# Kernel optimization log

Measured on AMD Instinct MI355X. Metric: run time of the kernel, lower is better.

## Reference

```python
import jax, jax.numpy as jnp
import numpy as np
from math import sqrt


def setup_inputs() -> dict:
    key = jax.random.key(0)
    k1, k2, k3, k4, k5 = jax.random.split(key, 5)
    B, L, H, D = 16, 4096, 16, 64
    S, M = 4096, 256
    queries = jax.random.normal(k1, (B, L, H, D), dtype=jnp.float32)
    keys = jax.random.normal(k2, (B, S, H, D), dtype=jnp.float32)
    values = jax.random.normal(k3, (B, S, H, D), dtype=jnp.float32)
    # nn.Linear(L_k=S, M): weight [M, S], bias [M]
    squeeze_w = jax.random.normal(k4, (M, S), dtype=jnp.float32) / sqrt(S)
    squeeze_b = jax.random.normal(k5, (M,), dtype=jnp.float32) * 0.01
    return {"queries": queries, "keys": keys, "values": values,
            "squeeze_w": squeeze_w, "squeeze_b": squeeze_b}


def reference(queries, keys, values, squeeze_w, squeeze_b):
    # queries: [B,L,H,D]; keys/values: [B,S,H,D]; squeeze_w: [M,S]; squeeze_b: [M]
    B, L, H, D = queries.shape
    scale = 1.0 / sqrt(D)
    bias = squeeze_b[None, :, None, None]  # broadcast over [B,M,H,D]
    # Linear over the sequence axis S -> M (Linformer compression)
    keys_sq = jnp.einsum('bshd,ms->bmhd', keys, squeeze_w) + bias      # [B,M,H,D]
    values_sq = jnp.einsum('bshd,ms->bmhd', values, squeeze_w) + bias  # [B,M,H,D]
    # Scaled dot-product attention against compressed K/V
    attn = jnp.einsum('blhd,bmhd->bhlm', queries, keys_sq) * scale     # [B,H,L,M]
    attn = jax.nn.softmax(attn, axis=-1)  # dropout is identity in eval / p=0
    context = jnp.einsum('bhlm,bmhd->blhd', attn, values_sq)           # [B,L,H,D]
    return context
```

## Files before the change

kernel.cpp:

```cpp
#include <hip/hip_runtime.h>

#define NB 16
#define NL 4096
#define NH 16
#define ND 64
#define NS 4096
#define NM 256

typedef __fp16 f16;
typedef __attribute__((ext_vector_type(8)))  __fp16 f16x8;
typedef __attribute__((ext_vector_type(4)))  __fp16 f16x4;
typedef __attribute__((ext_vector_type(2)))  __fp16 f16x2;
typedef __attribute__((ext_vector_type(4)))  float  f32x4;
typedef __attribute__((ext_vector_type(16))) float  f32x16;

__device__ __forceinline__ void gload_lds16(const void* g, void* l) {
  __builtin_amdgcn_global_load_lds(
      (const __attribute__((address_space(1))) void*)g,
      (__attribute__((address_space(3))) void*)l, 16, 0, 0);
}

__device__ __forceinline__ int pk2(float a, float b) {
  f16x2 t = __builtin_amdgcn_cvt_pkrtz(a, b);
  union { f16x2 h; int i; } u; u.h = t; return u.i;
}

__global__ __launch_bounds__(256) void k_wcvt(const float* __restrict__ W,
                                              f16* __restrict__ Wk) {
  const int o  = blockIdx.x * 256 + threadIdx.x;
  const int m  = o & 255;
  const int kb = o >> 8;
  const float* src = W + (long)m * NS + kb * 8;
  f32x4 v0 = *(const f32x4*)(src);
  f32x4 v1 = *(const f32x4*)(src + 4);
  union { f16x8 v; f16x2 h2[4]; } pk;
  pk.h2[0] = __builtin_amdgcn_cvt_pkrtz(v0[0], v0[1]);
  pk.h2[1] = __builtin_amdgcn_cvt_pkrtz(v0[2], v0[3]);
  pk.h2[2] = __builtin_amdgcn_cvt_pkrtz(v1[0], v1[1]);
  pk.h2[3] = __builtin_amdgcn_cvt_pkrtz(v1[2], v1[3]);
  *(f16x8*)(Wk + (long)o * 8) = pk.v;
}

__global__ __launch_bounds__(512, 4) void k_squeeze_p(
    const f16* __restrict__ Wk, const float* __restrict__ keys,
    const float* __restrict__ values, float* __restrict__ P) {
  const int h  = blockIdx.x & 15;
  const int b  = (blockIdx.x >> 4) & 15;
  const int sq = (blockIdx.x >> 8) & 1;
  const int t  = blockIdx.x >> 9;
  const float* __restrict__ X = t ? values : keys;

  __shared__ __align__(16) f16 XT0[64 * 72];
  __shared__ __align__(16) f16 XT1[64 * 72];

  const int tid  = threadIdx.x;
  const int lane = tid & 63;
  const int w    = tid >> 6;
  const int l31  = lane & 31;
  const int g    = lane >> 5;

  const int sp = tid & 31;
  const int ng = tid >> 5;
  const float* Xb = X + ((long)b * NS + sq * 2048) * (NH * ND) + h * ND;

  f32x16 acc[2];
#pragma unroll
  for (int di = 0; di < 2; ++di)
#pragma unroll
    for (int r = 0; r < 16; ++r) acc[di][r] = 0.f;

  f32x4 xrA[2], xrB[2];
#pragma unroll
  for (int r = 0; r < 2; ++r)
    xrA[r] = *(const f32x4*)(Xb + (long)(2 * sp + r) * (NH * ND) + ng * 4);
#pragma unroll
  for (int r = 0; r < 2; ++r)
    xrB[r] = *(const f32x4*)(Xb + (long)(64 + 2 * sp + r) * (NH * ND) + ng * 4);

  const f16* Wlane = Wk + ((long)sq * 256 * 256 + (long)g * 256 + w * 32 + l31) * 8;

  for (int kt2 = 0; kt2 < 16; ++kt2) {
    {
      const int kt = 2 * kt2;
      f16x8 af[4];
#pragma unroll
      for (int ks = 0; ks < 4; ++ks)
        af[ks] = *(const f16x8*)(Wlane + ((long)(kt * 8 + ks * 2) * 256) * 8);
      int p0 = pk2(xrA[0][0], xrA[1][0]);
      int p1 = pk2(xrA[0][1], xrA[1][1]);
      int p2 = pk2(xrA[0][2], xrA[1][2]);
      int p3 = pk2(xrA[0][3], xrA[1][3]);
      if (kt2 < 15) {
#pragma unroll
        for (int r = 0; r < 2; ++r)
          xrA[r] = *(const f32x4*)(Xb + (long)((kt + 2) * 64 + 2 * sp + r) * (NH * ND) + ng * 4);
      }
      *(int*)((char*)XT0 + (ng * 4 + 0) * 144 + sp * 4) = p0;
      *(int*)((char*)XT0 + (ng * 4 + 1) * 144 + sp * 4) = p1;
      *(int*)((char*)XT0 + (ng * 4 + 2) * 144 + sp * 4) = p2;
      *(int*)((char*)XT0 + (ng * 4 + 3) * 144 + sp * 4) = p3;
      __syncthreads();
#pragma unroll
      for (int ks = 0; ks < 4; ++ks) {
        f16x8 bf0 = *(const f16x8*)((const char*)XT0 + l31 * 144 + ks * 32 + g * 16);
        f16x8 bf1 = *(const f16x8*)((const char*)XT0 + (32 + l31) * 144 + ks * 32 + g * 16);
        acc[0] = __builtin_amdgcn_mfma_f32_32x32x16_f16(af[ks], bf0, acc[0], 0, 0, 0);
        acc[1] = __builtin_amdgcn_mfma_f32_32x32x16_f16(af[ks], bf1, acc[1], 0, 0, 0);
      }
    }
    {
      const int kt = 2 * kt2 + 1;
      f16x8 af[4];
#pragma unroll
      for (int ks = 0; ks < 4; ++ks)
        af[ks] = *(const f16x8*)(Wlane + ((long)(kt * 8 + ks * 2) * 256) * 8);
      int p0 = pk2(xrB[0][0], xrB[1][0]);
      int p1 = pk2(xrB[0][1], xrB[1][1]);
      int p2 = pk2(xrB[0][2], xrB[1][2]);
      int p3 = pk2(xrB[0][3], xrB[1][3]);
      if (kt2 < 15) {
#pragma unroll
        for (int r = 0; r < 2; ++r)
          xrB[r] = *(const f32x4*)(Xb + (long)((kt + 2) * 64 + 2 * sp + r) * (NH * ND) + ng * 4);
      }
      *(int*)((char*)XT1 + (ng * 4 + 0) * 144 + sp * 4) = p0;
      *(int*)((char*)XT1 + (ng * 4 + 1) * 144 + sp * 4) = p1;
      *(int*)((char*)XT1 + (ng * 4 + 2) * 144 + sp * 4) = p2;
      *(int*)((char*)XT1 + (ng * 4 + 3) * 144 + sp * 4) = p3;
      __syncthreads();
#pragma unroll
      for (int ks = 0; ks < 4; ++ks) {
        f16x8 bf0 = *(const f16x8*)((const char*)XT1 + l31 * 144 + ks * 32 + g * 16);
        f16x8 bf1 = *(const f16x8*)((const char*)XT1 + (32 + l31) * 144 + ks * 32 + g * 16);
        acc[0] = __builtin_amdgcn_mfma_f32_32x32x16_f16(af[ks], bf0, acc[0], 0, 0, 0);
        acc[1] = __builtin_amdgcn_mfma_f32_32x32x16_f16(af[ks], bf1, acc[1], 0, 0, 0);
      }
    }
  }

  const long bh = b * 16 + h;
  float* Pb = P + (((long)t * 256 + bh) * 2 + sq) * (NM * ND);
#pragma unroll
  for (int di = 0; di < 2; ++di) {
    const int d = di * 32 + l31;
#pragma unroll
    for (int rq = 0; rq < 4; ++rq) {
      const int m0 = w * 32 + rq * 8 + g * 4;
      f32x4 st;
      st[0] = acc[di][rq * 4 + 0]; st[1] = acc[di][rq * 4 + 1];
      st[2] = acc[di][rq * 4 + 2]; st[3] = acc[di][rq * 4 + 3];
      *(f32x4*)(Pb + d * 256 + m0) = st;
    }
  }
}

__global__ __launch_bounds__(256) void k_reduce(const float* __restrict__ P,
                                                const float* __restrict__ bias,
                                                f16* __restrict__ Ksq,
                                                f16* __restrict__ Vsq) {
  const int bh = blockIdx.x & 255;
  const int t  = blockIdx.x >> 8;
  const float* P0 = P + (((long)t * 256 + bh) * 2 + 0) * (NM * ND);
  const float* P1 = P + (((long)t * 256 + bh) * 2 + 1) * (NM * ND);
  const int tid = threadIdx.x;

#pragma unroll
  for (int i = 0; i < 16; ++i) {
    const int v = i * 256 + tid;
    const int d = v >> 6;
    const int m = (v & 63) * 4;
    f32x4 a = *(const f32x4*)(P0 + d * 256 + m);
    f32x4 bv = *(const f32x4*)(P1 + d * 256 + m);
    f32x4 bb = *(const f32x4*)(bias + m);
    f32x4 s = a + bv + bb;
    if (t == 0) {
      f16* K = Ksq + (long)bh * (NM * ND);
#pragma unroll
      for (int j = 0; j < 4; ++j)
        K[((d >> 3) * 256 + m + j) * 8 + (d & 7)] = (f16)s[j];
    } else {
      f16* V = Vsq + (long)bh * (ND * NM);
      f16x2 q0 = __builtin_amdgcn_cvt_pkrtz(s[0], s[1]);
      f16x2 q1 = __builtin_amdgcn_cvt_pkrtz(s[2], s[3]);
      f16x4 pv; pv[0] = q0[0]; pv[1] = q0[1]; pv[2] = q1[0]; pv[3] = q1[1];
      *(f16x4*)(V + ((m >> 3) * 64 + d) * 8 + (m & 7)) = pv;
    }
  }
}

__global__ __launch_bounds__(256, 2) void k_attn(const float* __restrict__ Q,
                                                 const f16* __restrict__ Ksq,
                                                 const f16* __restrict__ Vsq,
                                                 float* __restrict__ Out) {
  const int xcd   = blockIdx.x & 7;
  const int local = blockIdx.x >> 3;
  const int bh    = xcd * 32 + (local >> 1);
  const int chunk = local & 1;
  const int b = bh >> 4, h = bh & 15;

  __shared__ __align__(16) f16 Klds[8 * 256 * 8];
  __shared__ __align__(16) f16 Vlds[32 * 64 * 8];

  const int tid = threadIdx.x, lane = tid & 63, w = tid >> 6;
  const int q = lane & 31, hi = lane >> 5;

  const float* Qlane = Q   + (((long)b * NL + q) * NH + h) * ND;
  float*       Olane = Out + (((long)b * NL + q) * NH + h) * ND;
  const float  c = 0.125f * 1.44269504088896f;

  f32x4 qv[8];
  {
    const float* qp = Qlane + (long)(chunk * 2048 + w * 32) * (NH * ND) + hi * 8;
#pragma unroll
    for (int kt = 0; kt < 4; ++kt) {
      qv[2 * kt]     = *(const f32x4*)(qp + kt * 16);
      qv[2 * kt + 1] = *(const f32x4*)(qp + kt * 16 + 4);
    }
  }

  {
    const f16* Kg = Ksq + (long)bh * 16384;
    const f16* Vg = Vsq + (long)bh * 16384;
#pragma unroll
    for (int i = 0; i < 8; ++i)
      gload_lds16(Kg + w * 4096 + i * 512 + lane * 8, (char*)Klds + w * 8192 + i * 1024);
#pragma unroll
    for (int i = 0; i < 8; ++i)
      gload_lds16(Vg + w * 4096 + i * 512 + lane * 8, (char*)Vlds + w * 8192 + i * 1024);
  }
  __syncthreads();

  for (int it = 0; it < 16; ++it) {
    const int row0 = chunk * 2048 + it * 128 + w * 32;

    union { f16x8 v; f16x2 h2[4]; } qb[4];
#pragma unroll
    for (int kt = 0; kt < 4; ++kt) {
      qb[kt].h2[0] = __builtin_amdgcn_cvt_pkrtz(qv[2 * kt][0], qv[2 * kt][1]);
      qb[kt].h2[1] = __builtin_amdgcn_cvt_pkrtz(qv[2 * kt][2], qv[2 * kt][3]);
      qb[kt].h2[2] = __builtin_amdgcn_cvt_pkrtz(qv[2 * kt + 1][0], qv[2 * kt + 1][1]);
      qb[kt].h2[3] = __builtin_amdgcn_cvt_pkrtz(qv[2 * kt + 1][2], qv[2 * kt + 1][3]);
    }

    if (it + 1 < 16) {
      const float* qp = Qlane + (long)(row0 + 128) * (NH * ND) + hi * 8;
#pragma unroll
      for (int kt = 0; kt < 4; ++kt) {
        qv[2 * kt]     = *(const f32x4*)(qp + kt * 16);
        qv[2 * kt + 1] = *(const f32x4*)(qp + kt * 16 + 4);
      }
    }

    f32x16 sa[8];
#pragma unroll
    for (int mf = 0; mf < 8; ++mf)
#pragma unroll
      for (int r = 0; r < 16; ++r) sa[mf][r] = 0.f;

#pragma unroll
    for (int kt = 0; kt < 4; ++kt) {
#pragma unroll
      for (int mf = 0; mf < 8; ++mf) {
        f16x8 ka = *(const f16x8*)((const char*)Klds +
                                   ((2 * kt + hi) * 256 + mf * 32 + q) * 16);
        sa[mf] = __builtin_amdgcn_mfma_f32_32x32x16_f16(ka, qb[kt].v, sa[mf], 0, 0, 0);
      }
    }

    f32x16 mm = sa[0];
#pragma unroll
    for (int mf = 1; mf < 8; ++mf)
#pragma unroll
      for (int r = 0; r < 16; ++r) mm[r] = fmaxf(mm[r], sa[mf][r]);
    float m8_0 = fmaxf(mm[0], mm[8]),  m8_1 = fmaxf(mm[1], mm[9]);
    float m8_2 = fmaxf(mm[2], mm[10]), m8_3 = fmaxf(mm[3], mm[11]);
    float m8_4 = fmaxf(mm[4], mm[12]), m8_5 = fmaxf(mm[5], mm[13]);
    float m8_6 = fmaxf(mm[6], mm[14]), m8_7 = fmaxf(mm[7], mm[15]);
    float mx = fmaxf(fmaxf(fmaxf(m8_0, m8_1), fmaxf(m8_2, m8_3)),
                     fmaxf(fmaxf(m8_4, m8_5), fmaxf(m8_6, m8_7)));
    mx = fmaxf(mx, __shfl_xor(mx, 32));

#pragma unroll
    for (int mf = 0; mf < 8; ++mf)
#pragma unroll
      for (int r = 0; r < 16; ++r)
        sa[mf][r] = __builtin_amdgcn_exp2f((sa[mf][r] - mx) * c);

    f32x16 t0 = sa[0] + sa[1];
    f32x16 t1 = sa[2] + sa[3];
    f32x16 t2 = sa[4] + sa[5];
    f32x16 t3 = sa[6] + sa[7];
    t0 = (t0 + t1) + (t2 + t3);
    float s8_0 = t0[0] + t0[8],  s8_1 = t0[1] + t0[9];
    float s8_2 = t0[2] + t0[10], s8_3 = t0[3] + t0[11];
    float s8_4 = t0[4] + t0[12], s8_5 = t0[5] + t0[13];
    float s8_6 = t0[6] + t0[14], s8_7 = t0[7] + t0[15];
    float sum = ((s8_0 + s8_1) + (s8_2 + s8_3)) + ((s8_4 + s8_5) + (s8_6 + s8_7));
    sum += __shfl_xor(sum, 32);
    const float inv = 1.0f / sum;

    f32x16 o[2];
#pragma unroll
    for (int df = 0; df < 2; ++df)
#pragma unroll
      for (int r = 0; r < 16; ++r) o[df][r] = 0.f;

#pragma unroll
    for (int t = 0; t < 16; ++t) {
      const int fp = t >> 1, s = t & 1;
      int a0 = pk2(sa[fp][8 * s + 0] * inv, sa[fp][8 * s + 1] * inv);
      int a1 = pk2(sa[fp][8 * s + 2] * inv, sa[fp][8 * s + 3] * inv);
      int b0 = pk2(sa[fp][8 * s + 4] * inv, sa[fp][8 * s + 5] * inv);
      int b1 = pk2(sa[fp][8 * s + 6] * inv, sa[fp][8 * s + 7] * inv);
      asm volatile("v_permlane32_swap_b32 %0, %1" : "+v"(a0), "+v"(b0));
      asm volatile("v_permlane32_swap_b32 %0, %1" : "+v"(a1), "+v"(b1));
      union { int w4[4]; f16x8 v; } pb;
      pb.w4[0] = a0; pb.w4[1] = a1; pb.w4[2] = b0; pb.w4[3] = b1;
#pragma unroll
      for (int df = 0; df < 2; ++df) {
        f16x8 va = *(const f16x8*)((const char*)Vlds +
                                   ((2 * t + hi) * 64 + df * 32 + q) * 16);
        o[df] = __builtin_amdgcn_mfma_f32_32x32x16_f16(va, pb.v, o[df], 0, 0, 0);
      }
    }

    float* op = Olane + (long)row0 * (NH * ND);
#pragma unroll
    for (int df = 0; df < 2; ++df)
#pragma unroll
      for (int rq = 0; rq < 4; ++rq) {
        f32x4 st;
        st[0] = o[df][rq * 4 + 0]; st[1] = o[df][rq * 4 + 1];
        st[2] = o[df][rq * 4 + 2]; st[3] = o[df][rq * 4 + 3];
        *(f32x4*)(op + df * 32 + rq * 8 + hi * 4) = st;
      }
  }
}

extern "C" void kernel_launch(void* const* d_in, const int* in_sizes, int n_in,
                              void* d_out, int out_size, void* d_ws, size_t ws_size,
                              hipStream_t stream) {
  const float* Qp   = (const float*)d_in[0];
  const float* Kp   = (const float*)d_in[1];
  const float* Vp   = (const float*)d_in[2];
  const float* Wp   = (const float*)d_in[3];
  const float* bp   = (const float*)d_in[4];
  float*       Outp = (float*)d_out;

  char* ws = (char*)d_ws;
  f16*   Wk  = (f16*)ws;
  f16*   Ksq = (f16*)(ws + (2l << 20));
  f16*   Vsq = (f16*)(ws + (10l << 20));
  float* P   = (float*)(ws + (18l << 20));

  hipLaunchKernelGGL(k_wcvt, dim3(512), dim3(256), 0, stream, Wp, Wk);
  hipLaunchKernelGGL(k_squeeze_p, dim3(1024), dim3(512), 0, stream, Wk, Kp, Vp, P);
  hipLaunchKernelGGL(k_reduce, dim3(512), dim3(256), 0, stream, P, bp, Ksq, Vsq);
  hipLaunchKernelGGL(k_attn, dim3(512), dim3(256), 0, stream, Qp, Ksq, Vsq, Outp);
}
```

Before: 349.5 us.

## Retile squeeze GEMM to cover four heads per block with swizzled LDS

The squeeze kernel now uses 1024-thread blocks, each computing a 256x256 output tile (4 heads x 64 dims) instead of one head. The W fragment each wave loads is reused across 4 MFMA N-fragments, and the X rows are read as contiguous 1 KB chunks. LDS tiles are XOR-swizzled to avoid bank conflicts, and a custom barrier waits only on LDS counters so global prefetches stay in flight. Only 256 blocks are launched and LDS use per block is larger, which lowers occupancy and parallelism. The intermediate P layout and the reduce kernel's indexing change to match.

```diff
diff --git a/kernel.cpp b/kernel.cpp
--- a/kernel.cpp
+++ b/kernel.cpp
@@ -23,6 +23,13 @@
 __device__ __forceinline__ int pk2(float a, float b) {
   f16x2 t = __builtin_amdgcn_cvt_pkrtz(a, b);
   union { f16x2 h; int i; } u; u.h = t; return u.i;
+}
+
+__device__ __forceinline__ void sync_nodrain() {
+  asm volatile("s_waitcnt lgkmcnt(0)" ::: "memory");
+  __builtin_amdgcn_sched_barrier(0);
+  __builtin_amdgcn_s_barrier();
+  __builtin_amdgcn_sched_barrier(0);
 }
 
 __global__ __launch_bounds__(256) void k_wcvt(const float* __restrict__ W,
@@ -41,115 +48,91 @@
   *(f16x8*)(Wk + (long)o * 8) = pk.v;
 }
 
-__global__ __launch_bounds__(512, 4) void k_squeeze_p(
+__global__ __launch_bounds__(1024, 4) void k_squeeze_p(
     const f16* __restrict__ Wk, const float* __restrict__ keys,
     const float* __restrict__ values, float* __restrict__ P) {
-  const int h  = blockIdx.x & 15;
-  const int b  = (blockIdx.x >> 4) & 15;
-  const int sq = (blockIdx.x >> 8) & 1;
-  const int t  = blockIdx.x >> 9;
+  const int sq = blockIdx.x & 1;
+  const int nt = (blockIdx.x >> 1) & 3;
+  const int b  = (blockIdx.x >> 3) & 15;
+  const int t  = blockIdx.x >> 7;
   const float* __restrict__ X = t ? values : keys;
 
-  __shared__ __align__(16) f16 XT0[64 * 72];
-  __shared__ __align__(16) f16 XT1[64 * 72];
-
-  const int tid  = threadIdx.x;
+  __shared__ __align__(16) f16 XT0[64 * 256];
+  __shared__ __align__(16) f16 XT1[64 * 256];
+
+  const int tid = threadIdx.x;
   const int lane = tid & 63;
-  const int w    = tid >> 6;
+  const int wid  = tid >> 6;
   const int l31  = lane & 31;
   const int g    = lane >> 5;
-
-  const int sp = tid & 31;
-  const int ng = tid >> 5;
-  const float* Xb = X + ((long)b * NS + sq * 2048) * (NH * ND) + h * ND;
-
-  f32x16 acc[2];
-#pragma unroll
-  for (int di = 0; di < 2; ++di)
-#pragma unroll
-    for (int r = 0; r < 16; ++r) acc[di][r] = 0.f;
-
-  f32x4 xrA[2], xrB[2];
-#pragma unroll
-  for (int r = 0; r < 2; ++r)
-    xrA[r] = *(const f32x4*)(Xb + (long)(2 * sp + r) * (NH * ND) + ng * 4);
-#pragma unroll
-  for (int r = 0; r < 2; ++r)
-    xrB[r] = *(const f32x4*)(Xb + (long)(64 + 2 * sp + r) * (NH * ND) + ng * 4);
-
-  const f16* Wlane = Wk + ((long)sq * 256 * 256 + (long)g * 256 + w * 32 + l31) * 8;
-
-  for (int kt2 = 0; kt2 < 16; ++kt2) {
-    {
-      const int kt = 2 * kt2;
-      f16x8 af[4];
-#pragma unroll
-      for (int ks = 0; ks < 4; ++ks)
-        af[ks] = *(const f16x8*)(Wlane + ((long)(kt * 8 + ks * 2) * 256) * 8);
-      int p0 = pk2(xrA[0][0], xrA[1][0]);
-      int p1 = pk2(xrA[0][1], xrA[1][1]);
-      int p2 = pk2(xrA[0][2], xrA[1][2]);
-      int p3 = pk2(xrA[0][3], xrA[1][3]);
-      if (kt2 < 15) {
-#pragma unroll
-        for (int r = 0; r < 2; ++r)
-          xrA[r] = *(const f32x4*)(Xb + (long)((kt + 2) * 64 + 2 * sp + r) * (NH * ND) + ng * 4);
-      }
-      *(int*)((char*)XT0 + (ng * 4 + 0) * 144 + sp * 4) = p0;
-      *(int*)((char*)XT0 + (ng * 4 + 1) * 144 + sp * 4) = p1;
-      *(int*)((char*)XT0 + (ng * 4 + 2) * 144 + sp * 4) = p2;
-      *(int*)((char*)XT0 + (ng * 4 + 3) * 144 + sp * 4) = p3;
-      __syncthreads();
-#pragma unroll
-      for (int ks = 0; ks < 4; ++ks) {
-        f16x8 bf0 = *(const f16x8*)((const char*)XT0 + l31 * 144 + ks * 32 + g * 16);
-        f16x8 bf1 = *(const f16x8*)((const char*)XT0 + (32 + l31) * 144 + ks * 32 + g * 16);
-        acc[0] = __builtin_amdgcn_mfma_f32_32x32x16_f16(af[ks], bf0, acc[0], 0, 0, 0);
-        acc[1] = __builtin_amdgcn_mfma_f32_32x32x16_f16(af[ks], bf1, acc[1], 0, 0, 0);
-      }
-    }
-    {
-      const int kt = 2 * kt2 + 1;
-      f16x8 af[4];
-#pragma unroll
-      for (int ks = 0; ks < 4; ++ks)
-        af[ks] = *(const f16x8*)(Wlane + ((long)(kt * 8 + ks * 2) * 256) * 8);
-      int p0 = pk2(xrB[0][0], xrB[1][0]);
-      int p1 = pk2(xrB[0][1], xrB[1][1]);
-      int p2 = pk2(xrB[0][2], xrB[1][2]);
-      int p3 = pk2(xrB[0][3], xrB[1][3]);
-      if (kt2 < 15) {
-#pragma unroll
-        for (int r = 0; r < 2; ++r)
-          xrB[r] = *(const f32x4*)(Xb + (long)((kt + 2) * 64 + 2 * sp + r) * (NH * ND) + ng * 4);
-      }
-      *(int*)((char*)XT1 + (ng * 4 + 0) * 144 + sp * 4) = p0;
-      *(int*)((char*)XT1 + (ng * 4 + 1) * 144 + sp * 4) = p1;
-      *(int*)((char*)XT1 + (ng * 4 + 2) * 144 + sp * 4) = p2;
-      *(int*)((char*)XT1 + (ng * 4 + 3) * 144 + sp * 4) = p3;
-      __syncthreads();
-#pragma unroll
-      for (int ks = 0; ks < 4; ++ks) {
-        f16x8 bf0 = *(const f16x8*)((const char*)XT1 + l31 * 144 + ks * 32 + g * 16);
-        f16x8 bf1 = *(const f16x8*)((const char*)XT1 + (32 + l31) * 144 + ks * 32 + g * 16);
-        acc[0] = __builtin_amdgcn_mfma_f32_32x32x16_f16(af[ks], bf0, acc[0], 0, 0, 0);
-        acc[1] = __builtin_amdgcn_mfma_f32_32x32x16_f16(af[ks], bf1, acc[1], 0, 0, 0);
-      }
-    }
-  }
-
-  const long bh = b * 16 + h;
-  float* Pb = P + (((long)t * 256 + bh) * 2 + sq) * (NM * ND);
-#pragma unroll
-  for (int di = 0; di < 2; ++di) {
-    const int d = di * 32 + l31;
-#pragma unroll
-    for (int rq = 0; rq < 4; ++rq) {
-      const int m0 = w * 32 + rq * 8 + g * 4;
+  const int wm   = wid & 7;
+  const int wn   = wid >> 3;
+
+  const int nc = tid & 31;
+  const int sp = tid >> 5;
+
+  const float* Xr = X + ((long)b * NS + sq * 2048 + 2 * sp) * (NH * ND) + nt * 256 + nc * 8;
+
+  f32x16 acc[4];
+#pragma unroll
+  for (int nf = 0; nf < 4; ++nf)
+#pragma unroll
+    for (int r = 0; r < 16; ++r) acc[nf][r] = 0.f;
+
+  f32x4 xe0 = *(const f32x4*)(Xr);
+  f32x4 xe1 = *(const f32x4*)(Xr + 4);
+  f32x4 xo0 = *(const f32x4*)(Xr + NH * ND);
+  f32x4 xo1 = *(const f32x4*)(Xr + NH * ND + 4);
+
+  const long kb0 = (long)sq * 256;
+
+  for (int kt = 0; kt < 32; ++kt) {
+    f16* xt = (kt & 1) ? XT1 : XT0;
+#pragma unroll
+    for (int c = 0; c < 4; ++c) {
+      const int n = 8 * nc + c;
+      const int wa = n * 32 + (sp ^ (((nc ^ c) & 7) << 2));
+      *(int*)((char*)xt + wa * 4) = pk2(xe0[c], xo0[c]);
+    }
+#pragma unroll
+    for (int c = 0; c < 4; ++c) {
+      const int n = 8 * nc + 4 + c;
+      const int wa = n * 32 + (sp ^ (((nc ^ (4 + c)) & 7) << 2));
+      *(int*)((char*)xt + wa * 4) = pk2(xe1[c], xo1[c]);
+    }
+    if (kt < 31) {
+      const float* Xn = Xr + (long)(kt + 1) * 64 * (NH * ND);
+      xe0 = *(const f32x4*)(Xn);
+      xe1 = *(const f32x4*)(Xn + 4);
+      xo0 = *(const f32x4*)(Xn + NH * ND);
+      xo1 = *(const f32x4*)(Xn + NH * ND + 4);
+    }
+    sync_nodrain();
+#pragma unroll
+    for (int ks = 0; ks < 4; ++ks) {
+      f16x8 af = *(const f16x8*)(Wk + ((kb0 + kt * 8 + ks * 2 + g) * 256 + wm * 32 + l31) * 8);
+#pragma unroll
+      for (int nf = 0; nf < 4; ++nf) {
+        const int n  = wn * 128 + nf * 32 + l31;
+        const int wa = n * 32 + ((ks * 8 + g * 4) ^ ((((n >> 3) ^ n) & 7) << 2));
+        f16x8 bf = *(const f16x8*)((const char*)xt + wa * 4);
+        acc[nf] = __builtin_amdgcn_mfma_f32_32x32x16_f16(af, bf, acc[nf], 0, 0, 0);
+      }
+    }
+    sync_nodrain();
+  }
+
+  float* Pb = P + ((((long)t * 16 + b) * 4 + nt) * 2 + sq) * 65536;
+#pragma unroll
+  for (int nf = 0; nf < 4; ++nf) {
+    const int n = wn * 128 + nf * 32 + l31;
+#pragma unroll
+    for (int q = 0; q < 4; ++q) {
+      const int m = wm * 32 + q * 8 + g * 4;
       f32x4 st;
-      st[0] = acc[di][rq * 4 + 0]; st[1] = acc[di][rq * 4 + 1];
-      st[2] = acc[di][rq * 4 + 2]; st[3] = acc[di][rq * 4 + 3];
-      *(f32x4*)(Pb + d * 256 + m0) = st;
+      st[0] = acc[nf][q * 4 + 0]; st[1] = acc[nf][q * 4 + 1];
+      st[2] = acc[nf][q * 4 + 2]; st[3] = acc[nf][q * 4 + 3];
+      *(f32x4*)(Pb + (long)n * 256 + m) = st;
     }
   }
 }
@@ -160,8 +143,10 @@
                                                 f16* __restrict__ Vsq) {
   const int bh = blockIdx.x & 255;
   const int t  = blockIdx.x >> 8;
-  const float* P0 = P + (((long)t * 256 + bh) * 2 + 0) * (NM * ND);
-  const float* P1 = P + (((long)t * 256 + bh) * 2 + 1) * (NM * ND);
+  const int b = bh >> 4, h = bh & 15;
+  const long base = ((((long)t * 16 + b) * 4 + (h >> 2)) * 2) * 65536 + (long)(h & 3) * 64 * 256;
+  const float* P0 = P + base;
+  const float* P1 = P + base + 65536;
   const int tid = threadIdx.x;
 
 #pragma unroll
@@ -169,8 +154,8 @@
     const int v = i * 256 + tid;
     const int d = v >> 6;
     const int m = (v & 63) * 4;
-    f32x4 a = *(const f32x4*)(P0 + d * 256 + m);
-    f32x4 bv = *(const f32x4*)(P1 + d * 256 + m);
+    f32x4 a  = *(const f32x4*)(P0 + (long)d * 256 + m);
+    f32x4 bv = *(const f32x4*)(P1 + (long)d * 256 + m);
     f32x4 bb = *(const f32x4*)(bias + m);
     f32x4 s = a + bv + bb;
     if (t == 0) {
@@ -354,7 +339,7 @@
   float* P   = (float*)(ws + (18l << 20));
 
   hipLaunchKernelGGL(k_wcvt, dim3(512), dim3(256), 0, stream, Wp, Wk);
-  hipLaunchKernelGGL(k_squeeze_p, dim3(1024), dim3(512), 0, stream, Wk, Kp, Vp, P);
+  hipLaunchKernelGGL(k_squeeze_p, dim3(256), dim3(1024), 0, stream, Wk, Kp, Vp, P);
   hipLaunchKernelGGL(k_reduce, dim3(512), dim3(256), 0, stream, P, bp, Ksq, Vsq);
   hipLaunchKernelGGL(k_attn, dim3(512), dim3(256), 0, stream, Qp, Ksq, Vsq, Outp);
 }
```

Measured after the change: 336.6 us. -3.7%, faster.
